# Performance work log

Measured on AMD Instinct MI355X. Metric: run time of the kernel, lower is better.

The kernel has to match this reference:

```python
import jax, jax.numpy as jnp
import numpy as np

NUM_HEADS = 8
WIN = 7  # local_window_size
HALF = WIN // 2


def setup_inputs() -> dict:
    key = jax.random.key(0)
    k1, k2, k3 = jax.random.split(key, 3)
    B, N, C = 1, 4096, 384  # N = T*H*W with T=4, H=W=32
    x = jax.random.normal(k1, (B, N, C), dtype=jnp.float32)
    w_qkv = jax.random.normal(k2, (C, 3 * C), dtype=jnp.float32) * 0.02
    w_proj = jax.random.normal(k3, (C, C), dtype=jnp.float32) * 0.02
    b_proj = jnp.zeros((C,), dtype=jnp.float32)
    return {"x": x, "w_qkv": w_qkv, "w_proj": w_proj, "b_proj": b_proj, "H": 32, "W": 32}


def _gather_windows(t):
    H, W = t.shape[3], t.shape[4]
    tp = jnp.pad(t, ((0, 0), (0, 0), (0, 0), (HALF, HALF), (HALF, HALF), (0, 0)))
    wins = [tp[:, :, :, dy:dy + H, dx:dx + W, :] for dy in range(WIN) for dx in range(WIN)]
    return jnp.stack(wins, axis=5)


def reference(x, w_qkv, w_proj, b_proj, H, W):
    B, N, C = x.shape
    nh, hd = NUM_HEADS, C // NUM_HEADS
    T = N // (H * W)
    scale = hd ** (-0.5)

    qkv = (x @ w_qkv).reshape(B, N, 3, nh, hd)
    # (B, nh, T, H, W, hd)
    q = qkv[:, :, 0].transpose(0, 2, 1, 3).reshape(B, nh, T, H, W, hd)
    k = qkv[:, :, 1].transpose(0, 2, 1, 3).reshape(B, nh, T, H, W, hd)
    v = qkv[:, :, 2].transpose(0, 2, 1, 3).reshape(B, nh, T, H, W, hd)

    kwin = _gather_windows(k)  # (B, nh, T, H, W, 49, hd); zeros at borders (NOT masked)
    vwin = _gather_windows(v)

    scores = jnp.einsum('bnthwd,bnthwkd->bnthwk', q, kwin) * scale
    attn = jax.nn.softmax(scores, axis=-1)  # zero-padded keys give score 0 -> weight exp(0)
    out = jnp.einsum('bnthwk,bnthwkd->bnthwd', attn, vwin)

    out = out.transpose(0, 2, 3, 4, 1, 5).reshape(B, N, C)
    return out @ w_proj + b_proj
```

## Files before the change

### kernel.cpp

```cpp
#include <hip/hip_runtime.h>
#include <hip/hip_bf16.h>
#include <math.h>

#define NH 8
#define HD 48
#define C_DIM 384
#define C3 1152

typedef unsigned short ushort_t;
typedef __attribute__((ext_vector_type(8))) short short8;
typedef __attribute__((ext_vector_type(4))) float f32x4;

__global__ __launch_bounds__(256) void split_bf16_kernel(const float* __restrict__ in,
                                                         ushort_t* __restrict__ hi,
                                                         ushort_t* __restrict__ lo,
                                                         int n4)
{
    const int i = blockIdx.x * 256 + threadIdx.x;
    if (i >= n4) return;
    const float4 v = ((const float4*)in)[i];
    const float f[4] = {v.x, v.y, v.z, v.w};
    ushort_t hb[4], lb[4];
    #pragma unroll
    for (int j = 0; j < 4; ++j) {
        __hip_bfloat16 h = __float2bfloat16(f[j]);
        __hip_bfloat16 l = __float2bfloat16(f[j] - __bfloat162float(h));
        hb[j] = *(ushort_t*)&h;
        lb[j] = *(ushort_t*)&l;
    }
    *(ushort4*)(hi + i * 4) = make_ushort4(hb[0], hb[1], hb[2], hb[3]);
    *(ushort4*)(lo + i * 4) = make_ushort4(lb[0], lb[1], lb[2], lb[3]);
}

__global__ __launch_bounds__(256) void split_wT_kernel(const float* __restrict__ w,
                                                       ushort_t* __restrict__ hiT,
                                                       ushort_t* __restrict__ loT,
                                                       int K, int N)
{
    const int idx = blockIdx.x * 256 + threadIdx.x;
    if (idx >= K * N) return;
    const int k = idx / N;
    const int n = idx - k * N;
    const float v = w[idx];
    __hip_bfloat16 h = __float2bfloat16(v);
    __hip_bfloat16 l = __float2bfloat16(v - __bfloat162float(h));
    hiT[n * K + k] = *(ushort_t*)&h;
    loT[n * K + k] = *(ushort_t*)&l;
}

__global__ __launch_bounds__(256) void gemm_mfma3(const ushort_t* __restrict__ Ah,
                                                  const ushort_t* __restrict__ Al,
                                                  const ushort_t* __restrict__ BhT,
                                                  const ushort_t* __restrict__ BlT,
                                                  const float* __restrict__ bias,
                                                  float* __restrict__ C,
                                                  int N, int K)
{
    __shared__ ushort_t sAh[128 * 40];
    __shared__ ushort_t sAl[128 * 40];
    __shared__ ushort_t sBh[64 * 40];
    __shared__ ushort_t sBl[64 * 40];

    const int tid = threadIdx.x;
    const int bm = blockIdx.x * 128;
    const int bn = blockIdx.y * 64;

    const int rowA = tid >> 2;
    const int slotA = (tid & 3) * 8;
    const int rowB = tid >> 2;
    const int slotB = (tid & 3) * 8;

    const ushort_t* gAh0 = Ah + (size_t)(bm + rowA) * K + slotA;
    const ushort_t* gAh1 = Ah + (size_t)(bm + rowA + 64) * K + slotA;
    const ushort_t* gAl0 = Al + (size_t)(bm + rowA) * K + slotA;
    const ushort_t* gAl1 = Al + (size_t)(bm + rowA + 64) * K + slotA;
    const ushort_t* gBh  = BhT + (size_t)(bn + rowB) * K + slotB;
    const ushort_t* gBl  = BlT + (size_t)(bn + rowB) * K + slotB;

    const int lane = tid & 63;
    const int wid = tid >> 6;
    const int wm = wid >> 1;
    const int wn = wid & 1;
    const int fr = lane & 15;
    const int kb = lane >> 4;
    const int aoff = (wm * 64 + fr) * 40 + kb * 8;
    const int boff = (wn * 32 + fr) * 40 + kb * 8;

    f32x4 acc[4][2] = {};

    for (int k0 = 0; k0 < K; k0 += 32) {
        const short8 va0 = *(const short8*)(gAh0 + k0);
        const short8 va1 = *(const short8*)(gAh1 + k0);
        const short8 vl0 = *(const short8*)(gAl0 + k0);
        const short8 vl1 = *(const short8*)(gAl1 + k0);
        const short8 vb0 = *(const short8*)(gBh + k0);
        const short8 vb1 = *(const short8*)(gBl + k0);
        *(short8*)&sAh[rowA * 40 + slotA]        = va0;
        *(short8*)&sAh[(rowA + 64) * 40 + slotA] = va1;
        *(short8*)&sAl[rowA * 40 + slotA]        = vl0;
        *(short8*)&sAl[(rowA + 64) * 40 + slotA] = vl1;
        *(short8*)&sBh[rowB * 40 + slotB]        = vb0;
        *(short8*)&sBl[rowB * 40 + slotB]        = vb1;
        __syncthreads();

        short8 ah[4], al[4], bh[2], bl[2];
        #pragma unroll
        for (int m = 0; m < 4; ++m) {
            ah[m] = *(const short8*)&sAh[aoff + m * 16 * 40];
            al[m] = *(const short8*)&sAl[aoff + m * 16 * 40];
        }
        #pragma unroll
        for (int n = 0; n < 2; ++n) {
            bh[n] = *(const short8*)&sBh[boff + n * 16 * 40];
            bl[n] = *(const short8*)&sBl[boff + n * 16 * 40];
        }
        #pragma unroll
        for (int m = 0; m < 4; ++m) {
            #pragma unroll
            for (int n = 0; n < 2; ++n) {
                acc[m][n] = __builtin_amdgcn_mfma_f32_16x16x32_bf16(ah[m], bh[n], acc[m][n], 0, 0, 0);
                acc[m][n] = __builtin_amdgcn_mfma_f32_16x16x32_bf16(ah[m], bl[n], acc[m][n], 0, 0, 0);
                acc[m][n] = __builtin_amdgcn_mfma_f32_16x16x32_bf16(al[m], bh[n], acc[m][n], 0, 0, 0);
            }
        }
        __syncthreads();
    }

    #pragma unroll
    for (int n = 0; n < 2; ++n) {
        const int col = bn + wn * 32 + n * 16 + fr;
        const float bv = bias ? bias[col] : 0.f;
        #pragma unroll
        for (int m = 0; m < 4; ++m) {
            const int r0 = bm + wm * 64 + m * 16 + kb * 4;
            #pragma unroll
            for (int r = 0; r < 4; ++r) {
                C[(size_t)(r0 + r) * N + col] = acc[m][n][r] + bv;
            }
        }
    }
}

__global__ __launch_bounds__(256) void gemm64(const float* __restrict__ A,
                                              const float* __restrict__ B,
                                              const float* __restrict__ bias,
                                              float* __restrict__ C,
                                              int M, int N, int K)
{
    __shared__ float As[64][17];
    __shared__ float Bs[16][64];

    const int tid = threadIdx.x;
    const int tx = tid & 15;
    const int ty = tid >> 4;
    const int bm = blockIdx.x * 64;
    const int bn = blockIdx.y * 64;
    const int arow = tid >> 2;
    const int acol = (tid & 3) << 2;
    const int brow = tid >> 4;
    const int bcol = (tid & 15) << 2;

    float acc[4][4] = {};

    for (int k0 = 0; k0 < K; k0 += 16) {
        const float4 a4 = *(const float4*)(A + (size_t)(bm + arow) * K + k0 + acol);
        const float4 b4 = *(const float4*)(B + (size_t)(k0 + brow) * N + bn + bcol);
        As[arow][acol + 0] = a4.x; As[arow][acol + 1] = a4.y;
        As[arow][acol + 2] = a4.z; As[arow][acol + 3] = a4.w;
        *(float4*)&Bs[brow][bcol] = b4;
        __syncthreads();
        #pragma unroll
        for (int kk = 0; kk < 16; ++kk) {
            const float a0 = As[ty * 4 + 0][kk];
            const float a1 = As[ty * 4 + 1][kk];
            const float a2 = As[ty * 4 + 2][kk];
            const float a3 = As[ty * 4 + 3][kk];
            const float4 b = *(const float4*)&Bs[kk][tx * 4];
            acc[0][0] = fmaf(a0, b.x, acc[0][0]); acc[0][1] = fmaf(a0, b.y, acc[0][1]);
            acc[0][2] = fmaf(a0, b.z, acc[0][2]); acc[0][3] = fmaf(a0, b.w, acc[0][3]);
            acc[1][0] = fmaf(a1, b.x, acc[1][0]); acc[1][1] = fmaf(a1, b.y, acc[1][1]);
            acc[1][2] = fmaf(a1, b.z, acc[1][2]); acc[1][3] = fmaf(a1, b.w, acc[1][3]);
            acc[2][0] = fmaf(a2, b.x, acc[2][0]); acc[2][1] = fmaf(a2, b.y, acc[2][1]);
            acc[2][2] = fmaf(a2, b.z, acc[2][2]); acc[2][3] = fmaf(a2, b.w, acc[2][3]);
            acc[3][0] = fmaf(a3, b.x, acc[3][0]); acc[3][1] = fmaf(a3, b.y, acc[3][1]);
            acc[3][2] = fmaf(a3, b.z, acc[3][2]); acc[3][3] = fmaf(a3, b.w, acc[3][3]);
        }
        __syncthreads();
    }

    float4 bb = {0.f, 0.f, 0.f, 0.f};
    if (bias) bb = *(const float4*)(bias + bn + tx * 4);
    #pragma unroll
    for (int i = 0; i < 4; ++i) {
        float4 o;
        o.x = acc[i][0] + bb.x; o.y = acc[i][1] + bb.y;
        o.z = acc[i][2] + bb.z; o.w = acc[i][3] + bb.w;
        *(float4*)(C + (size_t)(bm + ty * 4 + i) * N + bn + tx * 4) = o;
    }
}

#define KV_ELEMS (7 * 40 * 64)
#define KV_PAD   1088
__global__ __launch_bounds__(512) void local_attn_mfma(const float* __restrict__ qkv,
                                                       ushort_t* __restrict__ outHi,
                                                       ushort_t* __restrict__ outLo)
{
    __shared__ ushort_t sKV[KV_ELEMS + KV_PAD];
    __shared__ ushort_t sP[7 * 32 * 64];
    __shared__ ushort_t sQ[32 * 64];
    __shared__ float    sS[32 * 57];

    const int tid = threadIdx.x;
    const int b = blockIdx.x;
    const int t = b >> 8, h = (b >> 3) & 31, head = b & 7;
    const float scale = 0.14433756729740643f;

    for (int i = tid; i < (KV_ELEMS + KV_PAD) / 2; i += 512) ((unsigned int*)sKV)[i] = 0u;
    for (int i = tid; i < (7 * 32 * 64) / 2; i += 512) ((unsigned int*)sP)[i] = 0u;
    for (int i = tid; i < (32 * 64) / 2; i += 512) ((unsigned int*)sQ)[i] = 0u;
    __syncthreads();

    for (int i = tid; i < 32 * 48; i += 512) {
        const int d = i % 48, q = i / 48;
        const int n = (t << 10) | (h << 5) | q;
        const float v = qkv[(size_t)n * C3 + head * HD + d] * scale;
        __hip_bfloat16 bv = __float2bfloat16(v);
        sQ[q * 64 + (d ^ ((q & 7) << 3))] = *(ushort_t*)&bv;
    }
    for (int i = tid; i < 7 * 40 * 48; i += 512) {
        const int d = i % 48;
        const int rest = i / 48;
        const int slot = rest % 40, r = rest / 40;
        const int c = slot - 3, hk = h + r - 3;
        float v = 0.f;
        if ((unsigned)c < 32u && (unsigned)hk < 32u)
            v = qkv[(size_t)(((t << 10) | (hk << 5) | c)) * C3 + C_DIM + head * HD + d];
        __hip_bfloat16 bv = __float2bfloat16(v);
        sKV[(r * 40 + slot) * 64 + (d ^ ((slot & 7) << 3))] = *(ushort_t*)&bv;
    }
    __syncthreads();

    const int wv = tid >> 6, l = tid & 63, lr = l & 15, lc = l >> 4;

    if (wv < 7) {
        const int r = wv;
        short8 aq[2][2];
        #pragma unroll
        for (int fm = 0; fm < 2; ++fm) {
            const int q = fm * 16 + lr;
            aq[fm][0] = *(const short8*)&sQ[q * 64 + ((lc * 8) ^ ((q & 7) << 3))];
            aq[fm][1] = *(const short8*)&sQ[q * 64 + ((lc * 8 + 32) ^ ((q & 7) << 3))];
        }
        #pragma unroll
        for (int fn = 0; fn < 3; ++fn) {
            const int slot = fn * 16 + lr;
            const short8 b0 = *(const short8*)&sKV[(r * 40 + slot) * 64 + ((lc * 8) ^ ((slot & 7) << 3))];
            const short8 b1 = *(const short8*)&sKV[(r * 40 + slot) * 64 + ((lc * 8 + 32) ^ ((slot & 7) << 3))];
            f32x4 acc0 = {}, acc1 = {};
            acc0 = __builtin_amdgcn_mfma_f32_16x16x32_bf16(aq[0][0], b0, acc0, 0, 0, 0);
            acc0 = __builtin_amdgcn_mfma_f32_16x16x32_bf16(aq[0][1], b1, acc0, 0, 0, 0);
            acc1 = __builtin_amdgcn_mfma_f32_16x16x32_bf16(aq[1][0], b0, acc1, 0, 0, 0);
            acc1 = __builtin_amdgcn_mfma_f32_16x16x32_bf16(aq[1][1], b1, acc1, 0, 0, 0);
            #pragma unroll
            for (int reg = 0; reg < 4; ++reg) {
                const int q0 = lc * 4 + reg;
                const int dx0 = slot - q0;
                if (dx0 >= 0 && dx0 < 7) sS[q0 * 57 + r * 7 + dx0] = acc0[reg];
                const int q1 = 16 + lc * 4 + reg;
                const int dx1 = slot - q1;
                if (dx1 >= 0 && dx1 < 7) sS[q1 * 57 + r * 7 + dx1] = acc1[reg];
            }
        }
    }
    __syncthreads();

    if (tid >= 32) {
        for (int i = tid - 32; i < 7 * 48 * 40; i += 480) {
            const int dim = i % 48;
            const int rest = i / 48;
            const int slot = rest % 40, r = rest / 40;
            const int c = slot - 3, hk = h + r - 3;
            float v = 0.f;
            if ((unsigned)c < 32u && (unsigned)hk < 32u)
                v = qkv[(size_t)(((t << 10) | (hk << 5) | c)) * C3 + 2 * C_DIM + head * HD + dim];
            __hip_bfloat16 bv = __float2bfloat16(v);
            sKV[(r * 48 + dim) * 40 + slot] = *(ushort_t*)&bv;
        }
    } else {
        const int q = tid;
        float sv[49];
        #pragma unroll
        for (int j = 0; j < 49; ++j) sv[j] = sS[q * 57 + j];
        float mx = sv[0];
        #pragma unroll
        for (int j = 1; j < 49; ++j) mx = fmaxf(mx, sv[j]);
        float sum = 0.f;
        #pragma unroll
        for (int j = 0; j < 49; ++j) { sv[j] = __expf(sv[j] - mx); sum += sv[j]; }
        const float inv = 1.f / sum;
        #pragma unroll
        for (int j = 0; j < 49; ++j) {
            const int r = j / 7, dx = j % 7;
            const int slot = q + dx;
            __hip_bfloat16 bv = __float2bfloat16(sv[j] * inv);
            sP[(r * 32 + q) * 64 + (slot ^ ((q & 7) << 3))] = *(ushort_t*)&bv;
        }
    }
    __syncthreads();

    if (wv < 6) {
        const int fm = (wv >= 3) ? 1 : 0;
        const int fn = wv - fm * 3;
        const int q = fm * 16 + lr;
        const int dim = fn * 16 + lr;
        f32x4 acc = {};
        #pragma unroll
        for (int r = 0; r < 7; ++r) {
            const short8 a0 = *(const short8*)&sP[(r * 32 + q) * 64 + ((lc * 8) ^ ((q & 7) << 3))];
            const short8 a1 = *(const short8*)&sP[(r * 32 + q) * 64 + ((lc * 8 + 32) ^ ((q & 7) << 3))];
            const short8 b0 = *(const short8*)&sKV[(r * 48 + dim) * 40 + lc * 8];
            const short8 b1 = *(const short8*)&sKV[(r * 48 + dim) * 40 + lc * 8 + 32];
            acc = __builtin_amdgcn_mfma_f32_16x16x32_bf16(a0, b0, acc, 0, 0, 0);
            acc = __builtin_amdgcn_mfma_f32_16x16x32_bf16(a1, b1, acc, 0, 0, 0);
        }
        #pragma unroll
        for (int reg = 0; reg < 4; ++reg) {
            const int qq = fm * 16 + lc * 4 + reg;
            const int n = (t << 10) | (h << 5) | qq;
            const float o = acc[reg];
            __hip_bfloat16 hb = __float2bfloat16(o);
            __hip_bfloat16 lb = __float2bfloat16(o - __bfloat162float(hb));
            const size_t ob = (size_t)n * C_DIM + head * HD + dim;
            outHi[ob] = *(ushort_t*)&hb;
            outLo[ob] = *(ushort_t*)&lb;
        }
    }
}

__global__ __launch_bounds__(256) void local_attn16(const float* __restrict__ qkv,
                                                    float* __restrict__ out)
{
    const int tid = threadIdx.x;
    const int dlane = tid & 15;
    const int gid = blockIdx.x * 16 + (tid >> 4);
    const int head = gid & 7;
    const int n = gid >> 3;
    const int t = n >> 10;
    const int h = (n >> 5) & 31;
    const int w = n & 31;
    const float scale = 0.14433756729740643f;

    const float* qp = qkv + (size_t)n * C3 + head * HD;
    const float q0 = qp[dlane];
    const float q1 = qp[dlane + 16];
    const float q2 = qp[dlane + 32];

    const size_t base_k = (size_t)(C_DIM + head * HD);
    const size_t base_v = (size_t)(2 * C_DIM + head * HD);

    float s[49];
    #pragma unroll
    for (int p = 0; p < 49; ++p) {
        const int dy = p / 7, dx = p % 7;
        const int hk = h + dy - 3;
        const int wk = w + dx - 3;
        float sc = 0.f;
        if ((unsigned)hk < 32u && (unsigned)wk < 32u) {
            const int nk = (t << 10) | (hk << 5) | wk;
            const float* kp = qkv + (size_t)nk * C3 + base_k;
            float acc = q0 * kp[dlane];
            acc = fmaf(q1, kp[dlane + 16], acc);
            acc = fmaf(q2, kp[dlane + 32], acc);
            acc += __shfl_xor(acc, 1, 16);
            acc += __shfl_xor(acc, 2, 16);
            acc += __shfl_xor(acc, 4, 16);
            acc += __shfl_xor(acc, 8, 16);
            sc = acc * scale;
        }
        s[p] = sc;
    }

    float m = s[0];
    #pragma unroll
    for (int p = 1; p < 49; ++p) m = fmaxf(m, s[p]);
    float sum = 0.f;
    #pragma unroll
    for (int p = 0; p < 49; ++p) { s[p] = __expf(s[p] - m); sum += s[p]; }
    const float inv = 1.f / sum;

    float o0 = 0.f, o1 = 0.f, o2 = 0.f;
    #pragma unroll
    for (int p = 0; p < 49; ++p) {
        const int dy = p / 7, dx = p % 7;
        const int hk = h + dy - 3;
        const int wk = w + dx - 3;
        if ((unsigned)hk < 32u && (unsigned)wk < 32u) {
            const float wgt = s[p] * inv;
            const int nk = (t << 10) | (hk << 5) | wk;
            const float* vp = qkv + (size_t)nk * C3 + base_v;
            o0 = fmaf(wgt, vp[dlane],      o0);
            o1 = fmaf(wgt, vp[dlane + 16], o1);
            o2 = fmaf(wgt, vp[dlane + 32], o2);
        }
    }

    float* op = out + (size_t)n * C_DIM + head * HD;
    op[dlane]      = o0;
    op[dlane + 16] = o1;
    op[dlane + 32] = o2;
}

extern "C" void kernel_launch(void* const* d_in, const int* in_sizes, int n_in,
                              void* d_out, int out_size, void* d_ws, size_t ws_size,
                              hipStream_t stream)
{
    const float* x      = (const float*)d_in[0];
    const float* w_qkv  = (const float*)d_in[1];
    const float* w_proj = (const float*)d_in[2];
    const float* b_proj = (const float*)d_in[3];

    const int M = 4096;
    dim3 blk(256);

    const size_t NEED = 33226752;

    unsigned char* ws = (unsigned char*)d_ws;
    float* qkv = (float*)ws;
    float* att = (float*)(ws + 18874368);

    if (ws_size >= NEED) {
        ushort_t* Ah  = (ushort_t*)(ws + 25165824);
        ushort_t* Al  = (ushort_t*)(ws + 28311552);
        ushort_t* BhT = (ushort_t*)(ws + 31457280);
        ushort_t* BlT = (ushort_t*)(ws + 32342016);

        split_bf16_kernel<<<dim3(1536), blk, 0, stream>>>(x, Ah, Al, M * C_DIM / 4);
        split_wT_kernel<<<dim3((C_DIM * C3 + 255) / 256), blk, 0, stream>>>(w_qkv, BhT, BlT, C_DIM, C3);
        gemm_mfma3<<<dim3(M / 128, C3 / 64), blk, 0, stream>>>(Ah, Al, BhT, BlT, nullptr, qkv, C3, C_DIM);

        local_attn_mfma<<<dim3(1024), dim3(512), 0, stream>>>(qkv, Ah, Al);

        split_wT_kernel<<<dim3((C_DIM * C_DIM + 255) / 256), blk, 0, stream>>>(w_proj, BhT, BlT, C_DIM, C_DIM);
        gemm_mfma3<<<dim3(M / 128, C_DIM / 64), blk, 0, stream>>>(Ah, Al, BhT, BlT, b_proj, (float*)d_out, C_DIM, C_DIM);
    } else {
        gemm64<<<dim3(M / 64, C3 / 64), blk, 0, stream>>>(x, w_qkv, nullptr, qkv, M, C3, C_DIM);
        local_attn16<<<dim3(2048), blk, 0, stream>>>(qkv, att);
        gemm64<<<dim3(M / 64, C_DIM / 64), blk, 0, stream>>>(att, w_proj, b_proj, (float*)d_out, M, C_DIM, C_DIM);
    }
}
```

Measured before the change: 101.6 us.

## Restructure local attention kernel: prefetch V early, share K/P buffer, spread QK MFMA

The attention kernel now loads Q, K and V into shared memory in one upfront phase, with loops tiled for coalescing, instead of loading V during the softmax phase. This removes the serialized V load after the score computation. It also drops most of the full-buffer zero-fill passes. The QK^T MFMA work (21 tiles) is spread across all 8 waves rather than 7 waves each doing 3 tiles. The K buffer is reused for the unswizzled probability matrix (row stride 72), which needs an extra zero-fill and barrier, and the probability reads may hit more LDS bank conflicts.

Result: faster. 98.33 us (-3.2%).

```diff
diff --git a/kernel.cpp b/kernel.cpp
--- a/kernel.cpp
+++ b/kernel.cpp
@@ -199,15 +199,15 @@
     }
 }
 
-#define KV_ELEMS (7 * 40 * 64)
-#define KV_PAD   1088
-__global__ __launch_bounds__(512) void local_attn_mfma(const float* __restrict__ qkv,
-                                                       ushort_t* __restrict__ outHi,
-                                                       ushort_t* __restrict__ outLo)
-{
-    __shared__ ushort_t sKV[KV_ELEMS + KV_PAD];
-    __shared__ ushort_t sP[7 * 32 * 64];
-    __shared__ ushort_t sQ[32 * 64];
+#define KP_SHORTS 18432
+#define PROW 72
+__global__ __launch_bounds__(512) void local_attn_mfma2(const float* __restrict__ qkv,
+                                                        ushort_t* __restrict__ outHi,
+                                                        ushort_t* __restrict__ outLo)
+{
+    __shared__ ushort_t sKP[KP_SHORTS];
+    __shared__ ushort_t sV[13504];
+    __shared__ ushort_t sQ[2048];
     __shared__ float    sS[32 * 57];
 
     const int tid = threadIdx.x;
@@ -215,35 +215,59 @@
     const int t = b >> 8, h = (b >> 3) & 31, head = b & 7;
     const float scale = 0.14433756729740643f;
 
-    for (int i = tid; i < (KV_ELEMS + KV_PAD) / 2; i += 512) ((unsigned int*)sKV)[i] = 0u;
-    for (int i = tid; i < (7 * 32 * 64) / 2; i += 512) ((unsigned int*)sP)[i] = 0u;
-    for (int i = tid; i < (32 * 64) / 2; i += 512) ((unsigned int*)sQ)[i] = 0u;
-    __syncthreads();
-
-    for (int i = tid; i < 32 * 48; i += 512) {
-        const int d = i % 48, q = i / 48;
-        const int n = (t << 10) | (h << 5) | q;
-        const float v = qkv[(size_t)n * C3 + head * HD + d] * scale;
+    if (tid < 288) {
+        if (tid < 256) ((unsigned int*)(sKP + 17920))[tid] = 0u;
+        else           ((unsigned int*)(sV + 13440))[tid - 256] = 0u;
+    }
+
+    #pragma unroll
+    for (int it = 0; it < 4; ++it) {
+        const int i = tid + it * 512;
+        const int q = i >> 6, d = i & 63;
+        float v = 0.f;
+        if (d < 48)
+            v = qkv[(size_t)((t << 10) + (h << 5) + q) * C3 + head * HD + d] * scale;
         __hip_bfloat16 bv = __float2bfloat16(v);
         sQ[q * 64 + (d ^ ((q & 7) << 3))] = *(ushort_t*)&bv;
     }
-    for (int i = tid; i < 7 * 40 * 48; i += 512) {
-        const int d = i % 48;
-        const int rest = i / 48;
-        const int slot = rest % 40, r = rest / 40;
-        const int c = slot - 3, hk = h + r - 3;
-        float v = 0.f;
-        if ((unsigned)c < 32u && (unsigned)hk < 32u)
-            v = qkv[(size_t)(((t << 10) | (hk << 5) | c)) * C3 + C_DIM + head * HD + d];
-        __hip_bfloat16 bv = __float2bfloat16(v);
-        sKV[(r * 40 + slot) * 64 + (d ^ ((slot & 7) << 3))] = *(ushort_t*)&bv;
+    #pragma unroll
+    for (int r = 0; r < 7; ++r) {
+        const int hk = h + r - 3;
+        const bool rowok = (unsigned)hk < 32u;
+        const size_t rk = (size_t)((t << 10) + (hk << 5)) * C3 + C_DIM + head * HD;
+        #pragma unroll
+        for (int it = 0; it < 5; ++it) {
+            const int i = tid + it * 512;
+            const int slot = i >> 6, d = i & 63;
+            const int c = slot - 3;
+            float v = 0.f;
+            if (rowok && (unsigned)c < 32u && d < 48)
+                v = qkv[rk + (size_t)c * C3 + d];
+            __hip_bfloat16 bv = __float2bfloat16(v);
+            sKP[(r * 40 + slot) * 64 + (d ^ ((slot & 7) << 3))] = *(ushort_t*)&bv;
+        }
+    }
+    #pragma unroll
+    for (int r = 0; r < 7; ++r) {
+        const int hk = h + r - 3;
+        const bool rowok = (unsigned)hk < 32u;
+        const size_t rv = (size_t)((t << 10) + (hk << 5)) * C3 + 2 * C_DIM + head * HD;
+        for (int i = tid; i < 1920; i += 512) {
+            const int dim = i / 40;
+            const int slot = i - dim * 40;
+            const int c = slot - 3;
+            float v = 0.f;
+            if (rowok && (unsigned)c < 32u)
+                v = qkv[rv + (size_t)c * C3 + dim];
+            __hip_bfloat16 bv = __float2bfloat16(v);
+            sV[(r * 48 + dim) * 40 + slot] = *(ushort_t*)&bv;
+        }
     }
     __syncthreads();
 
     const int wv = tid >> 6, l = tid & 63, lr = l & 15, lc = l >> 4;
 
-    if (wv < 7) {
-        const int r = wv;
+    {
         short8 aq[2][2];
         #pragma unroll
         for (int fm = 0; fm < 2; ++fm) {
@@ -251,11 +275,11 @@
             aq[fm][0] = *(const short8*)&sQ[q * 64 + ((lc * 8) ^ ((q & 7) << 3))];
             aq[fm][1] = *(const short8*)&sQ[q * 64 + ((lc * 8 + 32) ^ ((q & 7) << 3))];
         }
-        #pragma unroll
-        for (int fn = 0; fn < 3; ++fn) {
+        for (int u = wv; u < 21; u += 8) {
+            const int r = u / 3, fn = u - r * 3;
             const int slot = fn * 16 + lr;
-            const short8 b0 = *(const short8*)&sKV[(r * 40 + slot) * 64 + ((lc * 8) ^ ((slot & 7) << 3))];
-            const short8 b1 = *(const short8*)&sKV[(r * 40 + slot) * 64 + ((lc * 8 + 32) ^ ((slot & 7) << 3))];
+            const short8 b0 = *(const short8*)&sKP[(r * 40 + slot) * 64 + ((lc * 8) ^ ((slot & 7) << 3))];
+            const short8 b1 = *(const short8*)&sKP[(r * 40 + slot) * 64 + ((lc * 8 + 32) ^ ((slot & 7) << 3))];
             f32x4 acc0 = {}, acc1 = {};
             acc0 = __builtin_amdgcn_mfma_f32_16x16x32_bf16(aq[0][0], b0, acc0, 0, 0, 0);
             acc0 = __builtin_amdgcn_mfma_f32_16x16x32_bf16(aq[0][1], b1, acc0, 0, 0, 0);
@@ -274,19 +298,12 @@
     }
     __syncthreads();
 
-    if (tid >= 32) {
-        for (int i = tid - 32; i < 7 * 48 * 40; i += 480) {
-            const int dim = i % 48;
-            const int rest = i / 48;
-            const int slot = rest % 40, r = rest / 40;
-            const int c = slot - 3, hk = h + r - 3;
-            float v = 0.f;
-            if ((unsigned)c < 32u && (unsigned)hk < 32u)
-                v = qkv[(size_t)(((t << 10) | (hk << 5) | c)) * C3 + 2 * C_DIM + head * HD + dim];
-            __hip_bfloat16 bv = __float2bfloat16(v);
-            sKV[(r * 48 + dim) * 40 + slot] = *(ushort_t*)&bv;
-        }
-    } else {
+    #pragma unroll
+    for (int it = 0; it < 16; ++it)
+        ((unsigned int*)sKP)[tid + it * 512] = 0u;
+    __syncthreads();
+
+    if (tid < 32) {
         const int q = tid;
         float sv[49];
         #pragma unroll
@@ -300,10 +317,9 @@
         const float inv = 1.f / sum;
         #pragma unroll
         for (int j = 0; j < 49; ++j) {
-            const int r = j / 7, dx = j % 7;
-            const int slot = q + dx;
+            const int r = j / 7, dx = j - (j / 7) * 7;
             __hip_bfloat16 bv = __float2bfloat16(sv[j] * inv);
-            sP[(r * 32 + q) * 64 + (slot ^ ((q & 7) << 3))] = *(ushort_t*)&bv;
+            sKP[(r * 32 + q) * PROW + q + dx] = *(ushort_t*)&bv;
         }
     }
     __syncthreads();
@@ -316,10 +332,10 @@
         f32x4 acc = {};
         #pragma unroll
         for (int r = 0; r < 7; ++r) {
-            const short8 a0 = *(const short8*)&sP[(r * 32 + q) * 64 + ((lc * 8) ^ ((q & 7) << 3))];
-            const short8 a1 = *(const short8*)&sP[(r * 32 + q) * 64 + ((lc * 8 + 32) ^ ((q & 7) << 3))];
-            const short8 b0 = *(const short8*)&sKV[(r * 48 + dim) * 40 + lc * 8];
-            const short8 b1 = *(const short8*)&sKV[(r * 48 + dim) * 40 + lc * 8 + 32];
+            const short8 a0 = *(const short8*)&sKP[(r * 32 + q) * PROW + lc * 8];
+            const short8 a1 = *(const short8*)&sKP[(r * 32 + q) * PROW + lc * 8 + 32];
+            const short8 b0 = *(const short8*)&sV[(r * 48 + dim) * 40 + lc * 8];
+            const short8 b1 = *(const short8*)&sV[(r * 48 + dim) * 40 + lc * 8 + 32];
             acc = __builtin_amdgcn_mfma_f32_16x16x32_bf16(a0, b0, acc, 0, 0, 0);
             acc = __builtin_amdgcn_mfma_f32_16x16x32_bf16(a1, b1, acc, 0, 0, 0);
         }
@@ -438,7 +454,7 @@
         split_wT_kernel<<<dim3((C_DIM * C3 + 255) / 256), blk, 0, stream>>>(w_qkv, BhT, BlT, C_DIM, C3);
         gemm_mfma3<<<dim3(M / 128, C3 / 64), blk, 0, stream>>>(Ah, Al, BhT, BlT, nullptr, qkv, C3, C_DIM);
 
-        local_attn_mfma<<<dim3(1024), dim3(512), 0, stream>>>(qkv, Ah, Al);
+        local_attn_mfma2<<<dim3(1024), dim3(512), 0, stream>>>(qkv, Ah, Al);
 
         split_wT_kernel<<<dim3((C_DIM * C_DIM + 255) / 256), blk, 0, stream>>>(w_proj, BhT, BlT, C_DIM, C_DIM);
         gemm_mfma3<<<dim3(M / 128, C_DIM / 64), blk, 0, stream>>>(Ah, Al, BhT, BlT, b_proj, (float*)d_out, C_DIM, C_DIM);
```
